# Kernel tuning notes

Measured on AMD Instinct MI355X. Metric: run time of the kernel, lower is better.

Reference implementation:

```python
import jax, jax.numpy as jnp
import numpy as np

N_HEADS = 16


def setup_inputs() -> dict:
    key = jax.random.key(0)
    ks = jax.random.split(key, 5)
    B, S, D = 4, 1024, 1024
    H = N_HEADS
    hs = D // H
    sc = 0.02
    return {
        "x": jax.random.normal(ks[0], (B, S, D), jnp.float32),
        "Wqkv": jax.random.normal(ks[1], (3 * D, D), jnp.float32) * sc,
        "Wout": jax.random.normal(ks[2], (D, D), jnp.float32) * sc,
        "Wpos": jax.random.normal(ks[3], (D, D), jnp.float32) * sc,
        "posn_vect_u": jnp.zeros((1, H, 1, hs), jnp.float32),
        "posn_vect_v": jnp.zeros((1, H, 1, hs), jnp.float32),
        "rel_embed": jax.random.normal(ks[4], (S, D), jnp.float32) * sc,
    }


def reference(x, Wqkv, Wout, Wpos, posn_vect_u, posn_vect_v, rel_embed):
    B, S, D = x.shape
    H = N_HEADS
    hs = D // H

    # qkv projection (torch Linear: y = x @ W.T), split into q,k,v
    qkv = x @ Wqkv.T  # [B,S,3D]
    q, k, v = jnp.split(qkv, 3, axis=-1)
    # [B,S,D] -> [B,H,S,hs]
    q = q.reshape(B, S, H, hs).transpose(0, 2, 1, 3)
    k = k.reshape(B, S, H, hs).transpose(0, 2, 1, 3)
    v = v.reshape(B, S, H, hs).transpose(0, 2, 1, 3)

    # content term: (q + u) @ k^T -> [B,H,S,S]
    attn_dots = jnp.einsum("bhqd,bhkd->bhqk", q + posn_vect_u, k)

    # relative position term (Transformer-XL style)
    rel = rel_embed[-S:] @ Wpos.T          # [S,D]
    rel = rel.T.reshape(H, hs, S)          # [H,hs,S]
    query_posn = jnp.einsum("bhqd,hdk->bhqk", q + posn_vect_v, rel)  # [B,H,S,S]

    # rel-shift gather: shifted[i,j] = query_posn[i, j - i + S - 1]
    i = jnp.arange(S)[:, None]
    j = jnp.arange(S)[None, :]
    idx = jnp.clip(j - i + S - 1, 0, S - 1)  # [S,S]; entries with j>i masked later
    shifted = jnp.take_along_axis(query_posn, idx[None, None], axis=-1)
    attn_dots = attn_dots + shifted

    # causal mask then scaled softmax (matches masked_fill then softmax(x/sqrt(hs)))
    causal = j > i  # [S,S] True above diagonal
    attn_dots = jnp.where(causal[None, None], -jnp.inf, attn_dots)
    scores = jax.nn.softmax(attn_dots / np.sqrt(hs).astype(np.float32), axis=-1)

    attn = jnp.einsum("bhqk,bhkd->bhqd", scores, v)  # [B,H,S,hs]
    out = attn.transpose(0, 2, 1, 3).reshape(B, S, D) @ Wout.T
    return out
```

## Files before the change

kernel.cpp:

```cpp
#include <hip/hip_runtime.h>

#define S_LEN 1024

typedef unsigned short u16;
using bf16x8 = __attribute__((ext_vector_type(8))) short;
using bf16x4 = __attribute__((ext_vector_type(4))) short;
using f32x4  = __attribute__((ext_vector_type(4))) float;
using u16x8  = __attribute__((ext_vector_type(8))) unsigned short;
using u16x4  = __attribute__((ext_vector_type(4))) unsigned short;

__device__ __forceinline__ float bf2f(u16 b) {
  unsigned int u = ((unsigned int)b) << 16;
  return __builtin_bit_cast(float, u);
}
__device__ __forceinline__ u16 f2bf(float f) {
  unsigned int u = __builtin_bit_cast(unsigned int, f);
  unsigned int r = u + 0x7fffu + ((u >> 16) & 1u);
  return (u16)(r >> 16);
}

using gas_p = const __attribute__((address_space(1))) void*;
using las_p = __attribute__((address_space(3))) void*;
__device__ __forceinline__ void gload16(const void* g, void* l) {
  __builtin_amdgcn_global_load_lds((gas_p)g, (las_p)l, 16, 0, 0);
}

__global__ __launch_bounds__(256) void cvt_all(const float* __restrict__ x,
    const float* __restrict__ wqkv, const float* __restrict__ wout,
    const float* __restrict__ wpos, const float* __restrict__ rel,
    u16* __restrict__ xb, u16* __restrict__ wqkvb, u16* __restrict__ woutb,
    u16* __restrict__ wposb, u16* __restrict__ relb) {
  int blk = blockIdx.x;
  const float* src; u16* dst; int base;
  if (blk < 4096)      { src = x;    dst = xb;    base = blk; }
  else if (blk < 7168) { src = wqkv; dst = wqkvb; base = blk - 4096; }
  else if (blk < 8192) { src = wout; dst = woutb; base = blk - 7168; }
  else if (blk < 9216) { src = wpos; dst = wposb; base = blk - 8192; }
  else                 { src = rel;  dst = relb;  base = blk - 9216; }
  int i = (base * 256 + threadIdx.x) * 4;
  float4 v = *(const float4*)(src + i);
  u16x4 o;
  o.x = f2bf(v.x); o.y = f2bf(v.y); o.z = f2bf(v.z); o.w = f2bf(v.w);
  *(u16x4*)(dst + i) = o;
}

template <int MODE, int SWZ, int BM64>
__global__ __launch_bounds__(256) void gemm_bt(const u16* __restrict__ A,
    const u16* __restrict__ W, float* __restrict__ Yf, u16* __restrict__ Yb,
    u16* __restrict__ qc, u16* __restrict__ qp,
    const float* __restrict__ uvec, const float* __restrict__ vvec,
    int M, int N, int K) {
  constexpr int BM = BM64 ? 64 : 128;
  constexpr int MI = BM64 ? 2 : 4;
  __shared__ __align__(16) u16 As[2][BM * 32];
  __shared__ __align__(16) u16 Ws[2][128 * 32];
  const int t = threadIdx.x;
  const int w = t >> 6, l = t & 63;
  const int lr = l & 15, lg = l >> 4;
  int bm, bn;
  if (SWZ == 1) {
    int flat = (int)blockIdx.y * 32 + (int)blockIdx.x;
    int xcd = flat & 7, idx = flat >> 3;
    bm = (xcd & 3) * 8 + (idx & 7);
    bn = (xcd >> 2) * 12 + (idx >> 3);
  } else {
    bm = blockIdx.x; bn = blockIdx.y;
  }
  const int wr = BM64 ? ((w >> 1) * 32) : ((w >> 1) * 64);
  const int wc = (w & 1) * 64;
  f32x4 acc[MI][4];
#pragma unroll
  for (int mi = 0; mi < MI; ++mi)
#pragma unroll
    for (int ni = 0; ni < 4; ++ni) acc[mi][ni] = (f32x4){0.f, 0.f, 0.f, 0.f};
  const u16* Ab = A + (size_t)bm * BM * K;
  const u16* Wb = W + (size_t)bn * 128 * K;

  auto stage = [&](int k0, int buf) {
#pragma unroll
    for (int i = 0; i < (BM64 ? 1 : 2); ++i) {
      int c = i * 256 + t;
      gload16(Ab + (size_t)(c >> 2) * K + k0 + (c & 3) * 8, &As[buf][c * 8]);
    }
#pragma unroll
    for (int i = 0; i < 2; ++i) {
      int c = i * 256 + t;
      gload16(Wb + (size_t)(c >> 2) * K + k0 + (c & 3) * 8, &Ws[buf][c * 8]);
    }
  };

  stage(0, 0);
  __syncthreads();
  for (int k0 = 0; k0 < K; k0 += 32) {
    const int cur = (k0 >> 5) & 1;
    if (k0 + 32 < K) stage(k0 + 32, cur ^ 1);
    bf16x8 af[MI], wf[4];
#pragma unroll
    for (int mi = 0; mi < MI; ++mi)
      af[mi] = *(const bf16x8*)&As[cur][(wr + mi * 16 + lr) * 32 + lg * 8];
#pragma unroll
    for (int ni = 0; ni < 4; ++ni)
      wf[ni] = *(const bf16x8*)&Ws[cur][(wc + ni * 16 + lr) * 32 + lg * 8];
    __builtin_amdgcn_s_setprio(1);
#pragma unroll
    for (int mi = 0; mi < MI; ++mi)
#pragma unroll
      for (int ni = 0; ni < 4; ++ni)
        acc[mi][ni] = __builtin_amdgcn_mfma_f32_16x16x32_bf16(af[mi], wf[ni], acc[mi][ni], 0, 0, 0);
    __builtin_amdgcn_s_setprio(0);
    __syncthreads();
  }
#pragma unroll
  for (int mi = 0; mi < MI; ++mi)
#pragma unroll
    for (int ni = 0; ni < 4; ++ni) {
      int col = bn * 128 + wc + ni * 16 + lr;
      float uu = 0.f, vv = 0.f;
      if (MODE == 2 && col < 1024) { uu = uvec[col]; vv = vvec[col]; }
#pragma unroll
      for (int g = 0; g < 4; ++g) {
        int row = bm * BM + wr + mi * 16 + lg * 4 + g;
        float val = acc[mi][ni][g];
        if (MODE == 1) {
          Yf[(size_t)row * N + col] = val;
        } else if (MODE == 0) {
          Yb[(size_t)row * N + col] = f2bf(val);
        } else {
          if (col < 1024) {
            qc[(size_t)row * 1024 + col] = f2bf((val + uu) * 0.125f);
            qp[(size_t)row * 1024 + col] = f2bf((val + vv) * 0.125f);
          } else {
            Yb[(size_t)row * 3072 + col] = f2bf(val);
          }
        }
      }
    }
}

__global__ __launch_bounds__(256) void attn_fwd(
    const u16* __restrict__ qcb, const u16* __restrict__ qpb,
    const u16* __restrict__ qkv, const u16* __restrict__ relp,
    u16* __restrict__ out) {
  __shared__ __align__(16) u16 Ksb[2][4096];
  __shared__ __align__(16) u16 Vtb[2][4096];
  __shared__ __align__(16) u16 Rs3[3][4096];
  __shared__ __align__(16) float Psf[4][16][68];

  const int flat = (int)blockIdx.y * 8 + (int)blockIdx.x;
  const int wg = (flat & 7) * 64 + (flat >> 3);
  const int sub = wg & 7;
  const int bh = wg >> 3;
  const int b = bh >> 4, h = bh & 15;
  const int t = threadIdx.x;
  const int w = t >> 6, l = t & 63;
  const int lr = l & 15, lg = l >> 4;

  const u16* Kg = qkv + (size_t)b * S_LEN * 3072 + 1024 + h * 64;
  const u16* Vg = qkv + (size_t)b * S_LEN * 3072 + 2048 + h * 64;
  const u16* Rg = relp + h * 64;

  int gl4[4], cg[4];
#pragma unroll
  for (int g = 0; g < 4; ++g) {
    int ql = lg * 4 + g;
    gl4[g] = (l & 48) | ((lr - ql - 1) & 15);
    cg[g] = (lr > ql) ? 1 : 0;
  }

  for (int half = 0; half < 2; ++half) {
    const int qt = half ? sub : (15 - sub);
    const int i0 = qt * 64;
    const int nt = qt + 1;

    bf16x8 qcf[2], qpf[2];
    {
      size_t qoff = (size_t)(b * S_LEN + i0 + w * 16 + lr) * 1024 + h * 64;
      qcf[0] = *(const bf16x8*)(qcb + qoff + lg * 8);
      qcf[1] = *(const bf16x8*)(qcb + qoff + 32 + lg * 8);
      qpf[0] = *(const bf16x8*)(qpb + qoff + lg * 8);
      qpf[1] = *(const bf16x8*)(qpb + qoff + 32 + lg * 8);
    }

    auto stage_k = [&](int j0s, int buf) {
#pragma unroll
      for (int i = 0; i < 2; ++i) {
        int bK = i * 4 + w;
        int ttk = bK >> 1, kc = bK & 1;
        gload16(Kg + (size_t)(j0s + ttk * 16 + lr) * 3072 + kc * 32 + lg * 8,
                &Ksb[buf][bK * 512 + l * 8]);
      }
    };
    auto stage_rchunk = [&](int Gloc, int slot) {
      int Gg = 15 - qt + Gloc;
#pragma unroll
      for (int i = 0; i < 2; ++i) {
        int bR = i * 4 + w;
        int btc = bR >> 1, kc = bR & 1;
        int r = Gg * 64 + btc * 16 + lr;
        r = r > S_LEN - 1 ? S_LEN - 1 : r;
        gload16(Rg + (size_t)r * 1024 + kc * 32 + lg * 8,
                &Rs3[slot][bR * 512 + l * 8]);
      }
    };
    auto vload = [&](int j0s, u16x8* vv) {
#pragma unroll
      for (int i = 0; i < 2; ++i) {
        int c = i * 256 + t;
        vv[i] = *(const u16x8*)(Vg + (size_t)(j0s + (c >> 3)) * 3072 + (c & 7) * 8);
      }
    };
    auto vstore = [&](int buf, const u16x8* vv) {
#pragma unroll
      for (int i = 0; i < 2; ++i) {
        int c = i * 256 + t;
        int key = c >> 3;
        int d0 = (c & 7) * 8;
#pragma unroll
        for (int j = 0; j < 8; ++j) {
          int d = d0 + j;
          int blk = (d >> 4) * 2 + (key >> 5);
          int lane_s = ((key >> 3) & 3) * 16 + (d & 15);
          Vtb[buf][(blk * 64 + lane_s) * 8 + (key & 7)] = vv[i][j];
        }
      }
    };

    float m_run = -1e30f, l_run = 0.f;
    f32x4 o_acc[4];
#pragma unroll
    for (int dt = 0; dt < 4; ++dt) o_acc[dt] = (f32x4){0.f, 0.f, 0.f, 0.f};

    stage_k(0, 0);
    stage_rchunk(0, 0);
    stage_rchunk(1, 1);
    {
      u16x8 v0[2];
      vload(0, v0);
      vstore(0, v0);
    }
    __syncthreads();

    int sA = 0, sB = 1, sC = 2;
    for (int kt = 0; kt < nt; ++kt) {
      const int cur = kt & 1, nxt = cur ^ 1;
      const int j0 = kt * 64;
      const int have_nxt = (kt + 1 < nt);
      u16x8 vv[2];
      if (have_nxt) {
        stage_k(j0 + 64, nxt);
        stage_rchunk(kt + 2, sC);
        vload(j0 + 64, vv);
      }

      f32x4 sc[4];
      __builtin_amdgcn_s_setprio(1);
#pragma unroll
      for (int tt = 0; tt < 4; ++tt) {
        sc[tt] = (f32x4){0.f, 0.f, 0.f, 0.f};
#pragma unroll
        for (int kc = 0; kc < 2; ++kc) {
          bf16x8 kf = *(const bf16x8*)&Ksb[cur][(tt * 2 + kc) * 512 + l * 8];
          sc[tt] = __builtin_amdgcn_mfma_f32_16x16x32_bf16(qcf[kc], kf, sc[tt], 0, 0, 0);
        }
      }
      f32x4 sp[5];
#pragma unroll
      for (int u5 = 0; u5 < 5; ++u5) {
        int bt = 3 - w + u5;
        const u16* rb = (bt & 4) ? &Rs3[sB][0] : &Rs3[sA][0];
        int btc = bt & 3;
        sp[u5] = (f32x4){0.f, 0.f, 0.f, 0.f};
#pragma unroll
        for (int kc = 0; kc < 2; ++kc) {
          bf16x8 rf = *(const bf16x8*)&rb[(btc * 2 + kc) * 512 + l * 8];
          sp[u5] = __builtin_amdgcn_mfma_f32_16x16x32_bf16(qpf[kc], rf, sp[u5], 0, 0, 0);
        }
      }
      __builtin_amdgcn_s_setprio(0);

#pragma unroll
      for (int g = 0; g < 4; ++g) {
        float bp[5];
#pragma unroll
        for (int u5 = 0; u5 < 5; ++u5) bp[u5] = __shfl(sp[u5][g], gl4[g]);
        int ql = lg * 4 + g;
#pragma unroll
        for (int tt = 0; tt < 4; ++tt) {
          float band = cg[g] ? bp[tt + 1] : bp[tt];
          float z = sc[tt][g] + band;
          if (j0 + tt * 16 + lr > i0 + w * 16 + ql) z = -1e30f;
          Psf[w][ql][tt * 16 + lr] = z;
        }
      }

      float zz[2][8];
#pragma unroll
      for (int kc = 0; kc < 2; ++kc)
#pragma unroll
        for (int h4 = 0; h4 < 2; ++h4) {
          float4 rr = *(const float4*)&Psf[w][lr][kc * 32 + lg * 8 + h4 * 4];
          zz[kc][h4 * 4 + 0] = rr.x; zz[kc][h4 * 4 + 1] = rr.y;
          zz[kc][h4 * 4 + 2] = rr.z; zz[kc][h4 * 4 + 3] = rr.w;
        }
      float mt = zz[0][0];
#pragma unroll
      for (int kc = 0; kc < 2; ++kc)
#pragma unroll
        for (int j = 0; j < 8; ++j) mt = fmaxf(mt, zz[kc][j]);
      mt = fmaxf(mt, __shfl_xor(mt, 16));
      mt = fmaxf(mt, __shfl_xor(mt, 32));
      float mnew = fmaxf(m_run, mt);
      float corr = __expf(m_run - mnew);
      m_run = mnew;
      float s = 0.f;
#pragma unroll
      for (int kc = 0; kc < 2; ++kc)
#pragma unroll
        for (int j = 0; j < 8; ++j) {
          float e = __expf(zz[kc][j] - mnew);
          zz[kc][j] = e;
          s += e;
        }
      s += __shfl_xor(s, 16);
      s += __shfl_xor(s, 32);
      l_run = l_run * corr + s;

      float co[4];
#pragma unroll
      for (int g = 0; g < 4; ++g) co[g] = __shfl(corr, lg * 4 + g);
#pragma unroll
      for (int dt = 0; dt < 4; ++dt)
#pragma unroll
        for (int g = 0; g < 4; ++g) o_acc[dt][g] *= co[g];

      bf16x8 pf[2];
#pragma unroll
      for (int kc = 0; kc < 2; ++kc)
#pragma unroll
        for (int j = 0; j < 8; ++j) pf[kc][j] = (short)f2bf(zz[kc][j]);

      __builtin_amdgcn_s_setprio(1);
#pragma unroll
      for (int dt = 0; dt < 4; ++dt) {
#pragma unroll
        for (int kc = 0; kc < 2; ++kc) {
          bf16x8 vf = *(const bf16x8*)&Vtb[cur][(dt * 2 + kc) * 512 + l * 8];
          o_acc[dt] = __builtin_amdgcn_mfma_f32_16x16x32_bf16(pf[kc], vf, o_acc[dt], 0, 0, 0);
        }
      }
      __builtin_amdgcn_s_setprio(0);
      if (have_nxt) vstore(nxt, vv);
      __syncthreads();
      int stmp = sA; sA = sB; sB = sC; sC = stmp;
    }

    float ll[4];
#pragma unroll
    for (int g = 0; g < 4; ++g) ll[g] = __shfl(l_run, lg * 4 + g);
#pragma unroll
    for (int dt = 0; dt < 4; ++dt) {
      int col = h * 64 + dt * 16 + lr;
#pragma unroll
      for (int g = 0; g < 4; ++g) {
        int row = b * S_LEN + i0 + w * 16 + lg * 4 + g;
        out[(size_t)row * 1024 + col] = f2bf(o_acc[dt][g] / ll[g]);
      }
    }
  }
}

extern "C" void kernel_launch(void* const* d_in, const int* in_sizes, int n_in,
                              void* d_out, int out_size, void* d_ws, size_t ws_size,
                              hipStream_t stream) {
  const float* x    = (const float*)d_in[0];
  const float* Wqkv = (const float*)d_in[1];
  const float* Wout = (const float*)d_in[2];
  const float* Wpos = (const float*)d_in[3];
  const float* u    = (const float*)d_in[4];
  const float* v    = (const float*)d_in[5];
  const float* rel  = (const float*)d_in[6];
  float* out = (float*)d_out;

  u16* ws      = (u16*)d_ws;
  u16* xb      = ws;
  u16* wqkvb   = xb + 4194304;
  u16* woutb   = wqkvb + 3145728;
  u16* wposb   = woutb + 1048576;
  u16* relb    = wposb + 1048576;
  u16* qkvb    = relb + 1048576;
  u16* qcb     = qkvb + 12582912;
  u16* qpb     = qcb + 4194304;
  u16* relproj = qpb + 4194304;
  u16* attno   = relproj + 1048576;

  cvt_all<<<10240, 256, 0, stream>>>(x, Wqkv, Wout, Wpos, rel, xb, wqkvb, woutb, wposb, relb);

  gemm_bt<2, 1, 0><<<dim3(32, 24), 256, 0, stream>>>(xb, wqkvb, nullptr, qkvb, qcb, qpb, u, v, 4096, 3072, 1024);
  gemm_bt<0, 0, 1><<<dim3(16, 8), 256, 0, stream>>>(relb, wposb, nullptr, relproj, nullptr, nullptr, nullptr, nullptr, 1024, 1024, 1024);
  attn_fwd<<<dim3(8, 64), 256, 0, stream>>>(qcb, qpb, qkvb, relproj, attno);
  gemm_bt<1, 0, 1><<<dim3(64, 8), 256, 0, stream>>>(attno, woutb, out, nullptr, nullptr, nullptr, nullptr, nullptr, 4096, 1024, 1024);
}
```

Baseline: 151.1 us.

## Write V transposed from QKV GEMM epilogue and stage it with async LDS loads

The QKV projection epilogue now writes the V slice in a per-(batch,head) transposed layout (head dim major, keys contiguous) inside the qkv buffer. The attention kernel can then load V tiles straight into LDS with global_load_lds, the same way it loads K, in place of register loads followed by a scalar scatter into a transposed LDS layout. This removes the per-element LDS scatter and the register staging from the inner loop, and lets V loads overlap asynchronously. The cost is scattered 8-byte stores in the GEMM epilogue for the V columns.

```diff
diff --git a/kernel.cpp b/kernel.cpp
--- a/kernel.cpp
+++ b/kernel.cpp
@@ -4,7 +4,6 @@
 
 typedef unsigned short u16;
 using bf16x8 = __attribute__((ext_vector_type(8))) short;
-using bf16x4 = __attribute__((ext_vector_type(4))) short;
 using f32x4  = __attribute__((ext_vector_type(4))) float;
 using u16x8  = __attribute__((ext_vector_type(8))) unsigned short;
 using u16x4  = __attribute__((ext_vector_type(4))) unsigned short;
@@ -115,23 +114,40 @@
 #pragma unroll
     for (int ni = 0; ni < 4; ++ni) {
       int col = bn * 128 + wc + ni * 16 + lr;
-      float uu = 0.f, vv = 0.f;
-      if (MODE == 2 && col < 1024) { uu = uvec[col]; vv = vvec[col]; }
-#pragma unroll
-      for (int g = 0; g < 4; ++g) {
-        int row = bm * BM + wr + mi * 16 + lg * 4 + g;
-        float val = acc[mi][ni][g];
-        if (MODE == 1) {
-          Yf[(size_t)row * N + col] = val;
-        } else if (MODE == 0) {
-          Yb[(size_t)row * N + col] = f2bf(val);
+      if (MODE == 1) {
+#pragma unroll
+        for (int g = 0; g < 4; ++g) {
+          int row = bm * BM + wr + mi * 16 + lg * 4 + g;
+          Yf[(size_t)row * N + col] = acc[mi][ni][g];
+        }
+      } else if (MODE == 0) {
+#pragma unroll
+        for (int g = 0; g < 4; ++g) {
+          int row = bm * BM + wr + mi * 16 + lg * 4 + g;
+          Yb[(size_t)row * N + col] = f2bf(acc[mi][ni][g]);
+        }
+      } else {
+        if (col < 1024) {
+          float uu = uvec[col], vv = vvec[col];
+#pragma unroll
+          for (int g = 0; g < 4; ++g) {
+            int row = bm * BM + wr + mi * 16 + lg * 4 + g;
+            qc[(size_t)row * 1024 + col] = f2bf((acc[mi][ni][g] + uu) * 0.125f);
+            qp[(size_t)row * 1024 + col] = f2bf((acc[mi][ni][g] + vv) * 0.125f);
+          }
+        } else if (col < 2048) {
+#pragma unroll
+          for (int g = 0; g < 4; ++g) {
+            int row = bm * BM + wr + mi * 16 + lg * 4 + g;
+            Yb[(size_t)row * 3072 + col] = f2bf(acc[mi][ni][g]);
+          }
         } else {
-          if (col < 1024) {
-            qc[(size_t)row * 1024 + col] = f2bf((val + uu) * 0.125f);
-            qp[(size_t)row * 1024 + col] = f2bf((val + vv) * 0.125f);
-          } else {
-            Yb[(size_t)row * 3072 + col] = f2bf(val);
-          }
+          int row0 = bm * BM + wr + mi * 16 + lg * 4;
+          int vrow = (row0 >> 10) * 1024 + (col - 2048);
+          u16x4 tmp;
+#pragma unroll
+          for (int g = 0; g < 4; ++g) tmp[g] = f2bf(acc[mi][ni][g]);
+          *(u16x4*)&Yb[(size_t)vrow * 3072 + (row0 & 1023)] = tmp;
         }
       }
     }
@@ -156,7 +172,7 @@
   const int lr = l & 15, lg = l >> 4;
 
   const u16* Kg = qkv + (size_t)b * S_LEN * 3072 + 1024 + h * 64;
-  const u16* Vg = qkv + (size_t)b * S_LEN * 3072 + 2048 + h * 64;
+  const u16* Vg = qkv + (size_t)bh * 64 * 3072;
   const u16* Rg = relp + h * 64;
 
   int gl4[4], cg[4];
@@ -190,6 +206,15 @@
                 &Ksb[buf][bK * 512 + l * 8]);
       }
     };
+    auto stage_v = [&](int j0s, int buf) {
+#pragma unroll
+      for (int i = 0; i < 2; ++i) {
+        int bV = i * 4 + w;
+        int dt = bV >> 1, kc = bV & 1;
+        gload16(Vg + (size_t)(dt * 16 + lr) * 3072 + j0s + kc * 32 + lg * 8,
+                &Vtb[buf][bV * 512 + l * 8]);
+      }
+    };
     auto stage_rchunk = [&](int Gloc, int slot) {
       int Gg = 15 - qt + Gloc;
 #pragma unroll
@@ -202,28 +227,6 @@
                 &Rs3[slot][bR * 512 + l * 8]);
       }
     };
-    auto vload = [&](int j0s, u16x8* vv) {
-#pragma unroll
-      for (int i = 0; i < 2; ++i) {
-        int c = i * 256 + t;
-        vv[i] = *(const u16x8*)(Vg + (size_t)(j0s + (c >> 3)) * 3072 + (c & 7) * 8);
-      }
-    };
-    auto vstore = [&](int buf, const u16x8* vv) {
-#pragma unroll
-      for (int i = 0; i < 2; ++i) {
-        int c = i * 256 + t;
-        int key = c >> 3;
-        int d0 = (c & 7) * 8;
-#pragma unroll
-        for (int j = 0; j < 8; ++j) {
-          int d = d0 + j;
-          int blk = (d >> 4) * 2 + (key >> 5);
-          int lane_s = ((key >> 3) & 3) * 16 + (d & 15);
-          Vtb[buf][(blk * 64 + lane_s) * 8 + (key & 7)] = vv[i][j];
-        }
-      }
-    };
 
     float m_run = -1e30f, l_run = 0.f;
     f32x4 o_acc[4];
@@ -231,13 +234,9 @@
     for (int dt = 0; dt < 4; ++dt) o_acc[dt] = (f32x4){0.f, 0.f, 0.f, 0.f};
 
     stage_k(0, 0);
+    stage_v(0, 0);
     stage_rchunk(0, 0);
     stage_rchunk(1, 1);
-    {
-      u16x8 v0[2];
-      vload(0, v0);
-      vstore(0, v0);
-    }
     __syncthreads();
 
     int sA = 0, sB = 1, sC = 2;
@@ -245,11 +244,10 @@
       const int cur = kt & 1, nxt = cur ^ 1;
       const int j0 = kt * 64;
       const int have_nxt = (kt + 1 < nt);
-      u16x8 vv[2];
       if (have_nxt) {
         stage_k(j0 + 64, nxt);
+        stage_v(j0 + 64, nxt);
         stage_rchunk(kt + 2, sC);
-        vload(j0 + 64, vv);
       }
 
       f32x4 sc[4];
@@ -349,7 +347,6 @@
         }
       }
       __builtin_amdgcn_s_setprio(0);
-      if (have_nxt) vstore(nxt, vv);
       __syncthreads();
       int stmp = sA; sA = sB; sB = sC; sC = stmp;
     }
```

Measured after the change: 138.6 us. 8.2% less time.
